# Performance work log

Hardware: AMD Instinct MI355X
Metric: run time of the kernel (lower is better)

Reference implementation:

```python
import jax, jax.numpy as jnp
import numpy as np

CODEBOOK_SIZE = 1024
LATENT_DIM = 64
BETA = 0.25      # commitment_beta
DECAY = 0.99     # ema_decay
EPS = 1e-5       # ema_eps
DIVERSITY_W = 1.0


def _hadamard(n):
    # Sylvester construction (n must be a power of 2)
    H = np.array([[1.0]], dtype=np.float32)
    while H.shape[0] < n:
        H = np.block([[H, H], [H, -H]])
    return H.astype(np.float32)


def setup_inputs() -> dict:
    key = jax.random.key(0)
    k1, k2, k3 = jax.random.split(key, 3)
    B, C, H, W = 32, LATENT_DIM, 32, 32
    x = jax.random.normal(k1, (B, C, H, W), dtype=jnp.float32)
    embedding_weight = jax.random.normal(k2, (CODEBOOK_SIZE, LATENT_DIM), dtype=jnp.float32)
    rotation_matrix = jnp.asarray(_hadamard(LATENT_DIM))
    ema_w = jax.random.normal(k3, (CODEBOOK_SIZE, LATENT_DIM), dtype=jnp.float32)
    ema_cluster_size = jnp.ones((CODEBOOK_SIZE,), dtype=jnp.float32)
    return {"x": x, "embedding_weight": embedding_weight,
            "rotation_matrix": rotation_matrix, "ema_w": ema_w,
            "ema_cluster_size": ema_cluster_size}


def reference(x, embedding_weight, rotation_matrix, ema_w, ema_cluster_size):
    B, C, H, W = x.shape
    K, D = embedding_weight.shape
    N = B * H * W
    sg = jax.lax.stop_gradient

    # flatten channel-last, rotate
    xf = jnp.transpose(x, (0, 2, 3, 1)).reshape(N, D)      # [N, D]
    xr = xf @ rotation_matrix                               # [N, D]

    # pairwise squared distances to codebook + argmin
    dist = (jnp.sum(xr * xr, axis=-1, keepdims=True)
            + jnp.sum(embedding_weight * embedding_weight, axis=-1)[None, :]
            - 2.0 * (xr @ embedding_weight.T))              # [N, K]
    idx = jnp.argmin(dist, axis=-1)                         # [N]

    # one-hot scatter equivalents (counts / dw) done with index scatter-add
    counts = jnp.zeros((K,), x.dtype).at[idx].add(1.0)      # encodings.sum(0)
    quant = embedding_weight[idx]                           # [N, D]
    # NOTE: original code views (B*H*W, C) row-major directly as (B, C, H, W)
    quant_out = quant.reshape(B, C, H, W)

    # EMA codebook update (training=True path)
    cs = ema_cluster_size * DECAY + (1.0 - DECAY) * counts
    n = jnp.sum(cs)
    cs = (cs + EPS) / (n + K * EPS) * n
    dw = jnp.zeros((K, D), x.dtype).at[idx].add(xr)         # encodings.T @ xr
    new_ema_w = ema_w * DECAY + (1.0 - DECAY) * dw
    new_embedding = new_ema_w / cs[:, None]

    commitment_loss = BETA * jnp.mean((sg(quant_out) - x) ** 2)
    codebook_loss = jnp.mean((quant_out - sg(x)) ** 2)

    # diversity: mean over ALL (i, j) pairs of ||e_i - xr_j||^2 (original
    # broadcasts (N,1,D) vs (N,D) -> (N,N,D)); identical closed form:
    e = new_embedding[idx]                                  # [N, D]
    diversity_loss = DIVERSITY_W * (jnp.mean(jnp.sum(e * e, axis=-1))
                                    + jnp.mean(jnp.sum(xr * xr, axis=-1))
                                    - 2.0 * jnp.dot(jnp.mean(e, axis=0), jnp.mean(xr, axis=0)))

    avg_probs = counts / N
    perplexity = jnp.exp(-jnp.sum(avg_probs * jnp.log(avg_probs + 1e-10)))

    quant_st = x + sg(quant_out - x)                        # straight-through
    return (quant_st, codebook_loss, commitment_loss, diversity_loss,
            perplexity, idx, cs, new_ema_w, new_embedding)
```

## Files before the change

kernel.cpp:

```cpp
#include <hip/hip_runtime.h>
#include <math.h>

#define NTOK 32768
#define KCB  1024
#define DIM  64
#define THETA 0.02f

typedef __attribute__((ext_vector_type(8))) short short8;
typedef __attribute__((ext_vector_type(4))) float f32x4;
#define MFMA __builtin_amdgcn_mfma_f32_16x16x32_bf16
#define ALOAD(p) __hip_atomic_load((p), __ATOMIC_RELAXED, __HIP_MEMORY_SCOPE_AGENT)

#define WS_XR      0
#define WS_ENORM   2097152
#define WS_EH      2098176
#define WS_EL      2130944
#define WS_COUNTS  2163712
#define WS_CS      2164736
#define WS_XRSUM   2165760
#define WS_ESUM    2166272
#define WS_SCALREP 2166784
#define WS_FLAGCNT 2166912
#define WS_IDX     2166928
#define WS_FLAG    2199696
#define WS_SORT    2232464
#define WS_OFF     2265232
#define WS_CUR     2266256

#define O_Q    0
#define O_CB   2097152
#define O_CM   2097153
#define O_DV   2097154
#define O_PP   2097155
#define O_IDX  2097156
#define O_CS   2129924
#define O_EW   2130948
#define O_EMB  2196484

__device__ __forceinline__ void hilo(float v, unsigned &h, unsigned &l)
{
    unsigned b  = __float_as_uint(v);
    unsigned hb = (b + 0x7FFFu + ((b >> 16) & 1u)) & 0xFFFF0000u;
    float lof   = v - __uint_as_float(hb);
    unsigned lb = __float_as_uint(lof);
    l = (lb + 0x7FFFu + ((lb >> 16) & 1u)) >> 16;
    h = hb >> 16;
}

__global__ __launch_bounds__(256) void k_rotate_enorm(const float* __restrict__ x,
    const float* __restrict__ E, float* __restrict__ xr, float* __restrict__ enorm,
    unsigned short* __restrict__ eh, unsigned short* __restrict__ el,
    float* __restrict__ counts, int* __restrict__ flagc)
{
    int tid = threadIdx.x;
    if (blockIdx.x >= 512) {
        int b = (int)blockIdx.x - 512;
        counts[(b << 8) + tid] = 0.f;
        if (b == 0 && tid < 16) flagc[tid] = 0;
        int k = (b << 8) + tid;
        const float* ep = E + ((size_t)k << 6);
        unsigned* ehw = (unsigned*)eh + (k << 5);
        unsigned* elw = (unsigned*)el + (k << 5);
        float s = 0.f;
        #pragma unroll
        for (int q = 0; q < 32; ++q) {
            float v0 = ep[2*q], v1 = ep[2*q+1];
            s = fmaf(v0, v0, s); s = fmaf(v1, v1, s);
            unsigned h0, l0, h1, l1;
            hilo(v0, h0, l0);
            hilo(v1, h1, l1);
            ehw[q] = h0 | (h1 << 16);
            elw[q] = l0 | (l1 << 16);
        }
        enorm[k] = s;
        return;
    }
    __shared__ float xt[64 * 65];
    int p  = blockIdx.x >> 4;
    int s0 = ((int)blockIdx.x & 15) << 6;

    {
        const float4* x4 = (const float4*)x;
        #pragma unroll
        for (int pass = 0; pass < 4; ++pass) {
            int q = (pass << 8) + tid;
            int c = q >> 4, col = (q & 15) << 2;
            float4 v = x4[(p << 14) + (c << 8) + (s0 >> 2) + (col >> 2)];
            float* dst = xt + c * 65 + col;
            dst[0] = v.x; dst[1] = v.y; dst[2] = v.z; dst[3] = v.w;
        }
    }
    __syncthreads();

    int lane = tid & 63, w = tid >> 6;
    #pragma unroll
    for (int i = 0; i < 4; ++i) {
        int sl = (w << 4) + (i << 2);
        const float* src = xt + lane * 65 + sl;
        float4 v = make_float4(src[0], src[1], src[2], src[3]);
        #pragma unroll
        for (int s = 1; s <= 32; s <<= 1) {
            float sgn = (lane & s) ? -1.f : 1.f;
            float ox = __shfl_xor(v.x, s);
            float oy = __shfl_xor(v.y, s);
            float oz = __shfl_xor(v.z, s);
            float ow = __shfl_xor(v.w, s);
            v.x = fmaf(sgn, v.x, ox);
            v.y = fmaf(sgn, v.y, oy);
            v.z = fmaf(sgn, v.z, oz);
            v.w = fmaf(sgn, v.w, ow);
        }
        int t0 = ((int)blockIdx.x << 6) + sl;
        float* dst = xr + ((size_t)t0 << 6) + lane;
        dst[0]   = v.x;
        dst[64]  = v.y;
        dst[128] = v.z;
        dst[192] = v.w;
    }
}

__global__ __launch_bounds__(256, 4) void k_argmin(const float* __restrict__ xr,
    const unsigned short* __restrict__ eh, const unsigned short* __restrict__ el,
    const float* __restrict__ enorm, int* __restrict__ idxw,
    float* __restrict__ out_idx, float* __restrict__ counts,
    int* __restrict__ flagcnt, int* __restrict__ flaglist)
{
    __shared__ uint4 ehs[1024];
    __shared__ uint4 els[1024];
    __shared__ float ens[128];
    __shared__ float m_b1[32], m_b2[32];
    __shared__ int   m_id[32];
    int tid = threadIdx.x;
    int lane = tid & 63, w = tid >> 6;
    int ts = w >> 1, kh = w & 1;
    int tx = lane & 15, gq = lane >> 4;
    int tokbase = ((int)blockIdx.x << 5) + (ts << 4);

    short8 ah0, al0, ah1, al1;
    {
        const float* xp = xr + ((size_t)(tokbase + tx) << 6) + (gq << 3);
        float4 xa = *(const float4*)(xp);
        float4 xb = *(const float4*)(xp + 4);
        float4 xc = *(const float4*)(xp + 32);
        float4 xd = *(const float4*)(xp + 36);
        float a0v[8] = {xa.x,xa.y,xa.z,xa.w,xb.x,xb.y,xb.z,xb.w};
        float a1v[8] = {xc.x,xc.y,xc.z,xc.w,xd.x,xd.y,xd.z,xd.w};
        #pragma unroll
        for (int j = 0; j < 8; ++j) {
            unsigned h, l;
            hilo(a0v[j], h, l);
            ah0[j] = (short)h; al0[j] = (short)l;
            hilo(a1v[j], h, l);
            ah1[j] = (short)h; al1[j] = (short)l;
        }
    }

    float b1[4], b2[4]; int idx[4];
    #pragma unroll
    for (int r = 0; r < 4; ++r) { b1[r] = 3.4e38f; b2[r] = 3.4e38f; idx[r] = 0; }

    int swz0 = gq ^ (tx & 7);
    int swz1 = (4 + gq) ^ (tx & 7);
    const f32x4 z4 = {0.f, 0.f, 0.f, 0.f};

    for (int ch = 0; ch < 8; ++ch) {
        int c0 = ch << 7;
        __syncthreads();
        {
            const uint4* ghs = (const uint4*)eh + ((size_t)c0 << 3);
            const uint4* gls = (const uint4*)el + ((size_t)c0 << 3);
            #pragma unroll
            for (int i = 0; i < 4; ++i) {
                int u = (i << 8) + tid;
                int rr = u >> 3, bb = u & 7;
                int bs = bb ^ (rr & 7);
                ehs[(rr << 3) + bs] = ghs[u];
                els[(rr << 3) + bs] = gls[u];
            }
            if (tid < 128) ens[tid] = enorm[c0 + tid];
        }
        __syncthreads();

        #pragma unroll
        for (int s = 0; s < 4; ++s) {
            int rbase = (kh << 6) + (s << 4) + tx;
            short8 bh0 = ((const short8*)ehs)[(rbase << 3) + swz0];
            short8 bh1 = ((const short8*)ehs)[(rbase << 3) + swz1];
            short8 bl0 = ((const short8*)els)[(rbase << 3) + swz0];
            short8 bl1 = ((const short8*)els)[(rbase << 3) + swz1];

            f32x4 a0 = MFMA(ah0, bh0, z4, 0, 0, 0);
            a0 = MFMA(ah0, bl0, a0, 0, 0, 0);
            a0 = MFMA(al0, bh0, a0, 0, 0, 0);
            f32x4 a1 = MFMA(ah1, bh1, z4, 0, 0, 0);
            a1 = MFMA(ah1, bl1, a1, 0, 0, 0);
            a1 = MFMA(al1, bh1, a1, 0, 0, 0);

            float en = ens[rbase];
            int kk = c0 + rbase;
            #pragma unroll
            for (int r = 0; r < 4; ++r) {
                float sv = fmaf(-2.f, a0[r], fmaf(-2.f, a1[r], en));
                float mx = fmaxf(sv, b1[r]);
                b2[r] = fminf(b2[r], mx);
                bool t = sv < b1[r];
                idx[r] = t ? kk : idx[r];
                b1[r] = fminf(b1[r], sv);
            }
        }
    }

    float v1f[4], v2f[4]; int idf[4];
    #pragma unroll
    for (int r = 0; r < 4; ++r) {
        float v1 = b1[r], v2 = b2[r]; int id = idx[r];
        #pragma unroll
        for (int m = 1; m <= 8; m <<= 1) {
            float o1 = __shfl_xor(v1, m);
            float o2 = __shfl_xor(v2, m);
            int   oi = __shfl_xor(id, m);
            float nb2 = fminf(fminf(v2, o2), fmaxf(v1, o1));
            bool t = (o1 < v1) || (o1 == v1 && oi < id);
            v1 = t ? o1 : v1;
            id = t ? oi : id;
            v2 = nb2;
        }
        v1f[r] = v1; v2f[r] = v2; idf[r] = id;
    }

    int tl = (ts << 4) + (gq << 2);
    if (kh == 1 && tx == 0) {
        #pragma unroll
        for (int r = 0; r < 4; ++r) {
            m_b1[tl + r] = v1f[r];
            m_b2[tl + r] = v2f[r];
            m_id[tl + r] = idf[r];
        }
    }
    __syncthreads();
    if (kh == 0 && tx == 0) {
        #pragma unroll
        for (int r = 0; r < 4; ++r) {
            float o1 = m_b1[tl + r], o2 = m_b2[tl + r];
            int   oi = m_id[tl + r];
            float v1 = v1f[r]; int id = idf[r];
            float b2m = fminf(fminf(v2f[r], o2), fmaxf(v1, o1));
            bool t = (o1 < v1) || (o1 == v1 && oi < id);
            float v1m = t ? o1 : v1;
            int   idm = t ? oi : id;
            int tok = tokbase + (gq << 2) + r;
            idxw[tok] = idm;
            out_idx[tok] = (float)idm;
            atomicAdd(&counts[idm], 1.f);
            if (b2m - v1m < THETA) {
                int pz = atomicAdd(flagcnt, 1);
                flaglist[pz] = tok;
            }
        }
    }
}

__global__ __launch_bounds__(256) void k_fixup_scan(const float* __restrict__ xr,
    const float* __restrict__ E, const float* __restrict__ enorm,
    const float* __restrict__ ecs,
    const int* __restrict__ flagcnt, const int* __restrict__ flaglist,
    int* __restrict__ idxw, float* __restrict__ out_idx, float* __restrict__ counts,
    float* __restrict__ out_cs, float* __restrict__ csw,
    int* __restrict__ off, int* __restrict__ cur, int* __restrict__ done_ctr,
    float* __restrict__ e_sum, float* __restrict__ xr_sum,
    float* __restrict__ scalrep)
{
    int tid = threadIdx.x;
    int lane = tid & 63;
    int wid = ((int)blockIdx.x * 256 + tid) >> 6;
    int cnt = flagcnt[0];
    for (int i = wid; i < cnt; i += 512) {
        int tok = flaglist[i];
        const float4* xp = (const float4*)(xr + ((size_t)tok << 6));
        float4 xa[16];
        #pragma unroll
        for (int q = 0; q < 16; ++q) xa[q] = xp[q];
        float best = 3.4e38f; int bidx = 0;
        for (int c = 0; c < 16; ++c) {
            int k = (c << 6) + lane;
            const float4* epp = (const float4*)(E + ((size_t)k << 6));
            float d = 0.f;
            #pragma unroll
            for (int q = 0; q < 16; ++q) {
                float4 e = epp[q];
                d = fmaf(xa[q].x, e.x, d);
                d = fmaf(xa[q].y, e.y, d);
                d = fmaf(xa[q].z, e.z, d);
                d = fmaf(xa[q].w, e.w, d);
            }
            float sv = fmaf(-2.f, d, enorm[k]);
            if (sv < best) { best = sv; bidx = k; }
        }
        #pragma unroll
        for (int m = 1; m <= 32; m <<= 1) {
            float ov = __shfl_xor(best, m);
            int   oi = __shfl_xor(bidx, m);
            if (ov < best || (ov == best && oi < bidx)) { best = ov; bidx = oi; }
        }
        if (lane == 0) {
            int old = idxw[tok];
            if (old != bidx) {
                atomicAdd(&counts[old], -1.f);
                atomicAdd(&counts[bidx], 1.f);
                idxw[tok] = bidx;
                out_idx[tok] = (float)bidx;
            }
        }
    }

    __shared__ int ticket;
    __syncthreads();
    if (tid == 0) ticket = atomicAdd(done_ctr, 1);
    __syncthreads();
    if (ticket != 127) return;

    e_sum[tid]       = 0.f;
    e_sum[256 + tid] = 0.f;
    xr_sum[tid]       = 0.f;
    xr_sum[256 + tid] = 0.f;
    if (tid < 128) scalrep[tid] = 0.f;
    if (tid == 0) done_ctr[1] = 0;

    __shared__ float wsum2[4];
    __shared__ int   wcnt2[4], woff2[4];
    __shared__ float nss;
    int w = tid >> 6;
    float cs4[4]; int ci4[4];
    int s = 0; float csum = 0.f;
    #pragma unroll
    for (int j = 0; j < 4; ++j) {
        int kk = (tid << 2) + j;
        float c = ALOAD(&counts[kk]);
        float cs = ecs[kk] * 0.99f + 0.01f * c;
        cs4[j] = cs;
        ci4[j] = (int)c;
        s += ci4[j];
        csum += cs;
    }
    int sc = s;
    #pragma unroll
    for (int o = 1; o < 64; o <<= 1) {
        int u = __shfl_up(sc, o);
        if (lane >= o) sc += u;
    }
    float v = csum;
    #pragma unroll
    for (int m = 32; m >= 1; m >>= 1) v += __shfl_xor(v, m);
    if (lane == 63) wcnt2[w] = sc;
    if (lane == 0)  wsum2[w] = v;
    __syncthreads();
    if (tid == 0) {
        int run = 0;
        #pragma unroll
        for (int i = 0; i < 4; ++i) { woff2[i] = run; run += wcnt2[i]; }
        nss = wsum2[0] + wsum2[1] + wsum2[2] + wsum2[3];
    }
    __syncthreads();
    float nn = nss;
    int run = woff2[w] + (sc - s);
    #pragma unroll
    for (int j = 0; j < 4; ++j) {
        int kk = (tid << 2) + j;
        off[kk] = run;
        cur[kk] = run;
        run += ci4[j];
        float csf = (cs4[j] + 1e-5f) / (nn + 1024.f * 1e-5f) * nn;
        out_cs[kk] = csf;
        csw[kk] = csf;
    }
}

__global__ __launch_bounds__(256) void k_quantscatter(const float* __restrict__ x,
    const float* __restrict__ E, const int* __restrict__ idxw,
    int* __restrict__ cur, int* __restrict__ sorted,
    float* __restrict__ outq, float* __restrict__ scalrep)
{
    __shared__ int lidx[32];
    __shared__ float wr[4], wn[4];
    int tid = threadIdx.x;
    int n0 = (int)blockIdx.x << 5;
    if (tid < 32) {
        int k = idxw[n0 + tid];
        lidx[tid] = k;
        int pos = atomicAdd(&cur[k], 1);
        sorted[pos] = n0 + tid;
    }
    __syncthreads();
    int f40 = (int)blockIdx.x << 9;
    float sq = 0.f, xn = 0.f;
    #pragma unroll
    for (int it = 0; it < 2; ++it) {
        int q = (it << 8) + tid;
        int kk = lidx[q >> 4];
        int d4 = q & 15;
        float4 xv = ((const float4*)x)[f40 + q];
        float4 ev = ((const float4*)E)[(kk << 4) + d4];
        float dx = ev.x - xv.x, dy = ev.y - xv.y, dz = ev.z - xv.z, dw_ = ev.w - xv.w;
        ((float4*)outq)[f40 + q] = make_float4(xv.x + dx, xv.y + dy, xv.z + dz, xv.w + dw_);
        sq += dx*dx + dy*dy + dz*dz + dw_*dw_;
        xn += xv.x*xv.x + xv.y*xv.y + xv.z*xv.z + xv.w*xv.w;
    }
    #pragma unroll
    for (int m = 32; m >= 1; m >>= 1) { sq += __shfl_xor(sq, m); xn += __shfl_xor(xn, m); }
    if ((tid & 63) == 0) { wr[tid >> 6] = sq; wn[tid >> 6] = xn; }
    __syncthreads();
    if (tid == 0) {
        int rep = ((int)blockIdx.x & 7) << 4;
        atomicAdd(&scalrep[rep + 0], wr[0] + wr[1] + wr[2] + wr[3]);
        atomicAdd(&scalrep[rep + 1], wn[0] + wn[1] + wn[2] + wn[3]);
    }
}

__global__ __launch_bounds__(256) void k_dwemb_final(const float* __restrict__ xr,
    const int* __restrict__ sorted, const int* __restrict__ off,
    const float* __restrict__ counts, const float* __restrict__ csw,
    const float* __restrict__ emaw, float* __restrict__ out_ew,
    float* __restrict__ out_emb, float* __restrict__ e_sum,
    float* __restrict__ scalrep, float* __restrict__ xr_sum,
    float* __restrict__ out, int* __restrict__ done_ctr)
{
    __shared__ float part[3][64];
    int k = blockIdx.x;
    int tid = threadIdx.x;
    int w = tid >> 6, d = tid & 63;
    int a = off[k];
    int cnt = (int)counts[k];
    int end = a + cnt;

    float sum = 0.f;
    for (int t = a + w; t < end; t += 4) {
        int tok = sorted[t];
        sum += xr[((size_t)tok << 6) + d];
    }
    if (w) part[w - 1][d] = sum;
    __syncthreads();
    if (w == 0) {
        float dw = sum + part[0][d] + part[1][d] + part[2][d];
        int i = (k << 6) + d;
        float nw = emaw[i] * 0.99f + 0.01f * dw;
        out_ew[i] = nw;
        float emb = nw / csw[k];
        out_emb[i] = emb;
        if (cnt > 0) {
            int rep = (k & 7) << 6;
            atomicAdd(&xr_sum[rep + d], dw);
            float c = (float)cnt;
            atomicAdd(&e_sum[rep + d], c * emb);
            float t2 = c * emb * emb;
            #pragma unroll
            for (int m = 32; m >= 1; m >>= 1) t2 += __shfl_xor(t2, m);
            if (d == 0) atomicAdd(&scalrep[((k & 7) << 4) + 2], t2);
        }
    }

    __shared__ int ticket;
    __syncthreads();
    if (tid == 0) ticket = atomicAdd(done_ctr, 1);
    __syncthreads();
    if (ticket != 1023) return;

    __shared__ float wt[4], wd[4];
    float tt = 0.f;
    #pragma unroll
    for (int j = 0; j < 4; ++j) {
        float aa = ALOAD(&counts[(tid << 2) + j]) * (1.f / 32768.f);
        tt += aa * logf(aa + 1e-10f);
    }
    float dc = 0.f;
    if (tid < 64) {
        float xs8 = 0.f, es8 = 0.f;
        #pragma unroll
        for (int r2 = 0; r2 < 8; ++r2) {
            xs8 += ALOAD(&xr_sum[(r2 << 6) + tid]);
            es8 += ALOAD(&e_sum[(r2 << 6) + tid]);
        }
        dc = es8 * xs8;
    }
    #pragma unroll
    for (int m = 32; m >= 1; m >>= 1) { tt += __shfl_xor(tt, m); dc += __shfl_xor(dc, m); }
    if ((tid & 63) == 0) { wt[w] = tt; wd[w] = dc; }
    __syncthreads();
    if (tid == 0) {
        float S = wt[0] + wt[1] + wt[2] + wt[3];
        float Dt = wd[0] + wd[1] + wd[2] + wd[3];
        float sqs = 0.f, xns = 0.f, s2s = 0.f;
        #pragma unroll
        for (int r2 = 0; r2 < 8; ++r2) {
            sqs += scalrep[(r2 << 4) + 0];
            xns += scalrep[(r2 << 4) + 1];
            s2s += ALOAD(&scalrep[(r2 << 4) + 2]);
        }
        float cb = sqs * (1.f / 2097152.f);
        out[O_CB] = cb;
        out[O_CM] = 0.25f * cb;
        float inv = 1.f / 32768.f;
        out[O_DV] = s2s * inv + 64.f * xns * inv - 2.f * (Dt * inv * inv);
        out[O_PP] = expf(-S);
    }
}

extern "C" void kernel_launch(void* const* d_in, const int* in_sizes, int n_in,
                              void* d_out, int out_size, void* d_ws, size_t ws_size,
                              hipStream_t stream)
{
    const float* x    = (const float*)d_in[0];
    const float* E    = (const float*)d_in[1];
    const float* emaw = (const float*)d_in[3];
    const float* ecs  = (const float*)d_in[4];
    float* out = (float*)d_out;
    float* ws  = (float*)d_ws;
    int* flagc = (int*)(ws + WS_FLAGCNT);

    hipLaunchKernelGGL(k_rotate_enorm, dim3(516), dim3(256), 0, stream,
                       x, E, ws + WS_XR, ws + WS_ENORM,
                       (unsigned short*)(ws + WS_EH), (unsigned short*)(ws + WS_EL),
                       ws + WS_COUNTS, flagc);
    hipLaunchKernelGGL(k_argmin, dim3(1024), dim3(256), 0, stream,
                       ws + WS_XR, (const unsigned short*)(ws + WS_EH),
                       (const unsigned short*)(ws + WS_EL), ws + WS_ENORM,
                       (int*)(ws + WS_IDX), out + O_IDX, ws + WS_COUNTS,
                       flagc, (int*)(ws + WS_FLAG));
    hipLaunchKernelGGL(k_fixup_scan, dim3(128), dim3(256), 0, stream,
                       ws + WS_XR, E, ws + WS_ENORM, ecs,
                       flagc, (const int*)(ws + WS_FLAG),
                       (int*)(ws + WS_IDX), out + O_IDX, ws + WS_COUNTS,
                       out + O_CS, ws + WS_CS,
                       (int*)(ws + WS_OFF), (int*)(ws + WS_CUR), flagc + 1,
                       ws + WS_ESUM, ws + WS_XRSUM, ws + WS_SCALREP);
    hipLaunchKernelGGL(k_quantscatter, dim3(1024), dim3(256), 0, stream,
                       x, E, (const int*)(ws + WS_IDX), (int*)(ws + WS_CUR),
                       (int*)(ws + WS_SORT), out + O_Q, ws + WS_SCALREP);
    hipLaunchKernelGGL(k_dwemb_final, dim3(1024), dim3(256), 0, stream,
                       ws + WS_XR, (const int*)(ws + WS_SORT),
                       (const int*)(ws + WS_OFF), ws + WS_COUNTS, ws + WS_CS,
                       emaw, out + O_EW, out + O_EMB, ws + WS_ESUM,
                       ws + WS_SCALREP, ws + WS_XRSUM, out, flagc + 2);
}
```

Before: 116.8 us.

## Fuse fixup with quantize and scatter with dw kernel, cutting launches

Argmin now writes a per-token flag array instead of atomically appending to a flag list. The fixup pass is folded into the per-32-token quantize kernel, and a last-block ticket computes the cluster-size scan. The counting-sort scatter moves into the dw/embedding kernel, guarded by a grid-wide spin barrier. Accumulator zeroing moves into the first kernel. The goal is to remove one kernel launch and the serial 128-block fixup phase. The cost is a spin barrier that assumes all 1024 blocks are resident at once, which risks deadlock or stalls.

```diff
diff --git a/kernel.cpp b/kernel.cpp
--- a/kernel.cpp
+++ b/kernel.cpp
@@ -50,13 +50,22 @@
 __global__ __launch_bounds__(256) void k_rotate_enorm(const float* __restrict__ x,
     const float* __restrict__ E, float* __restrict__ xr, float* __restrict__ enorm,
     unsigned short* __restrict__ eh, unsigned short* __restrict__ el,
-    float* __restrict__ counts, int* __restrict__ flagc)
+    float* __restrict__ counts, int* __restrict__ flagc,
+    float* __restrict__ e_sum, float* __restrict__ xr_sum,
+    float* __restrict__ scalrep)
 {
     int tid = threadIdx.x;
     if (blockIdx.x >= 512) {
         int b = (int)blockIdx.x - 512;
         counts[(b << 8) + tid] = 0.f;
-        if (b == 0 && tid < 16) flagc[tid] = 0;
+        if (b == 0) {
+            if (tid < 16) flagc[tid] = 0;
+            if (tid < 128) scalrep[tid] = 0.f;
+        } else if (b == 1) {
+            e_sum[tid] = 0.f; e_sum[256 + tid] = 0.f;
+        } else if (b == 2) {
+            xr_sum[tid] = 0.f; xr_sum[256 + tid] = 0.f;
+        }
         int k = (b << 8) + tid;
         const float* ep = E + ((size_t)k << 6);
         unsigned* ehw = (unsigned*)eh + (k << 5);
@@ -123,7 +132,7 @@
     const unsigned short* __restrict__ eh, const unsigned short* __restrict__ el,
     const float* __restrict__ enorm, int* __restrict__ idxw,
     float* __restrict__ out_idx, float* __restrict__ counts,
-    int* __restrict__ flagcnt, int* __restrict__ flaglist)
+    int* __restrict__ flag)
 {
     __shared__ uint4 ehs[1024];
     __shared__ uint4 els[1024];
@@ -252,30 +261,42 @@
             idxw[tok] = idm;
             out_idx[tok] = (float)idm;
             atomicAdd(&counts[idm], 1.f);
-            if (b2m - v1m < THETA) {
-                int pz = atomicAdd(flagcnt, 1);
-                flaglist[pz] = tok;
-            }
+            flag[tok] = (b2m - v1m < THETA) ? 1 : 0;
         }
     }
 }
 
-__global__ __launch_bounds__(256) void k_fixup_scan(const float* __restrict__ xr,
-    const float* __restrict__ E, const float* __restrict__ enorm,
-    const float* __restrict__ ecs,
-    const int* __restrict__ flagcnt, const int* __restrict__ flaglist,
-    int* __restrict__ idxw, float* __restrict__ out_idx, float* __restrict__ counts,
+__global__ __launch_bounds__(256) void k_fixupquant_scan(const float* __restrict__ x,
+    const float* __restrict__ xr, const float* __restrict__ E,
+    const float* __restrict__ enorm, const float* __restrict__ ecs,
+    const int* __restrict__ flag, int* __restrict__ idxw,
+    float* __restrict__ out_idx, float* __restrict__ counts,
     float* __restrict__ out_cs, float* __restrict__ csw,
     int* __restrict__ off, int* __restrict__ cur, int* __restrict__ done_ctr,
-    float* __restrict__ e_sum, float* __restrict__ xr_sum,
-    float* __restrict__ scalrep)
+    float* __restrict__ outq, float* __restrict__ scalrep)
 {
+    __shared__ int lidx[32];
+    __shared__ unsigned fmask;
+    __shared__ float wr[4], wn[4];
     int tid = threadIdx.x;
-    int lane = tid & 63;
-    int wid = ((int)blockIdx.x * 256 + tid) >> 6;
-    int cnt = flagcnt[0];
-    for (int i = wid; i < cnt; i += 512) {
-        int tok = flaglist[i];
+    int lane = tid & 63, w = tid >> 6;
+    int n0 = (int)blockIdx.x << 5;
+
+    int fl = 0;
+    if (tid < 32) {
+        lidx[tid] = idxw[n0 + tid];
+        fl = flag[n0 + tid];
+    }
+    unsigned long long bal = __ballot(fl != 0);
+    if (tid == 0) fmask = (unsigned)bal;
+    __syncthreads();
+
+    unsigned msk = fmask;
+    int widx = 0;
+    while (msk) {
+        int src = __ffs(msk) - 1; msk &= msk - 1;
+        if ((widx++ & 3) != w) continue;
+        int tok = n0 + src;
         const float4* xp = (const float4*)(xr + ((size_t)tok << 6));
         float4 xa[16];
         #pragma unroll
@@ -303,94 +324,18 @@
             if (ov < best || (ov == best && oi < bidx)) { best = ov; bidx = oi; }
         }
         if (lane == 0) {
-            int old = idxw[tok];
+            int old = lidx[src];
             if (old != bidx) {
                 atomicAdd(&counts[old], -1.f);
                 atomicAdd(&counts[bidx], 1.f);
+                lidx[src] = bidx;
                 idxw[tok] = bidx;
                 out_idx[tok] = (float)bidx;
             }
         }
     }
-
-    __shared__ int ticket;
-    __syncthreads();
-    if (tid == 0) ticket = atomicAdd(done_ctr, 1);
-    __syncthreads();
-    if (ticket != 127) return;
-
-    e_sum[tid]       = 0.f;
-    e_sum[256 + tid] = 0.f;
-    xr_sum[tid]       = 0.f;
-    xr_sum[256 + tid] = 0.f;
-    if (tid < 128) scalrep[tid] = 0.f;
-    if (tid == 0) done_ctr[1] = 0;
-
-    __shared__ float wsum2[4];
-    __shared__ int   wcnt2[4], woff2[4];
-    __shared__ float nss;
-    int w = tid >> 6;
-    float cs4[4]; int ci4[4];
-    int s = 0; float csum = 0.f;
-    #pragma unroll
-    for (int j = 0; j < 4; ++j) {
-        int kk = (tid << 2) + j;
-        float c = ALOAD(&counts[kk]);
-        float cs = ecs[kk] * 0.99f + 0.01f * c;
-        cs4[j] = cs;
-        ci4[j] = (int)c;
-        s += ci4[j];
-        csum += cs;
-    }
-    int sc = s;
-    #pragma unroll
-    for (int o = 1; o < 64; o <<= 1) {
-        int u = __shfl_up(sc, o);
-        if (lane >= o) sc += u;
-    }
-    float v = csum;
-    #pragma unroll
-    for (int m = 32; m >= 1; m >>= 1) v += __shfl_xor(v, m);
-    if (lane == 63) wcnt2[w] = sc;
-    if (lane == 0)  wsum2[w] = v;
-    __syncthreads();
-    if (tid == 0) {
-        int run = 0;
-        #pragma unroll
-        for (int i = 0; i < 4; ++i) { woff2[i] = run; run += wcnt2[i]; }
-        nss = wsum2[0] + wsum2[1] + wsum2[2] + wsum2[3];
-    }
-    __syncthreads();
-    float nn = nss;
-    int run = woff2[w] + (sc - s);
-    #pragma unroll
-    for (int j = 0; j < 4; ++j) {
-        int kk = (tid << 2) + j;
-        off[kk] = run;
-        cur[kk] = run;
-        run += ci4[j];
-        float csf = (cs4[j] + 1e-5f) / (nn + 1024.f * 1e-5f) * nn;
-        out_cs[kk] = csf;
-        csw[kk] = csf;
-    }
-}
-
-__global__ __launch_bounds__(256) void k_quantscatter(const float* __restrict__ x,
-    const float* __restrict__ E, const int* __restrict__ idxw,
-    int* __restrict__ cur, int* __restrict__ sorted,
-    float* __restrict__ outq, float* __restrict__ scalrep)
-{
-    __shared__ int lidx[32];
-    __shared__ float wr[4], wn[4];
-    int tid = threadIdx.x;
-    int n0 = (int)blockIdx.x << 5;
-    if (tid < 32) {
-        int k = idxw[n0 + tid];
-        lidx[tid] = k;
-        int pos = atomicAdd(&cur[k], 1);
-        sorted[pos] = n0 + tid;
-    }
-    __syncthreads();
+    __syncthreads();
+
     int f40 = (int)blockIdx.x << 9;
     float sq = 0.f, xn = 0.f;
     #pragma unroll
@@ -407,34 +352,103 @@
     }
     #pragma unroll
     for (int m = 32; m >= 1; m >>= 1) { sq += __shfl_xor(sq, m); xn += __shfl_xor(xn, m); }
-    if ((tid & 63) == 0) { wr[tid >> 6] = sq; wn[tid >> 6] = xn; }
+    if (lane == 0) { wr[w] = sq; wn[w] = xn; }
     __syncthreads();
     if (tid == 0) {
         int rep = ((int)blockIdx.x & 7) << 4;
         atomicAdd(&scalrep[rep + 0], wr[0] + wr[1] + wr[2] + wr[3]);
         atomicAdd(&scalrep[rep + 1], wn[0] + wn[1] + wn[2] + wn[3]);
     }
+
+    __shared__ int ticket;
+    __syncthreads();
+    if (tid == 0) ticket = atomicAdd(done_ctr, 1);
+    __syncthreads();
+    if (ticket != 1023) return;
+
+    __shared__ float wsum2[4];
+    __shared__ int   wcnt2[4], woff2[4];
+    __shared__ float nss;
+    float cs4[4]; int ci4[4];
+    int s = 0; float csum = 0.f;
+    #pragma unroll
+    for (int j = 0; j < 4; ++j) {
+        int kk = (tid << 2) + j;
+        float c = ALOAD(&counts[kk]);
+        float cs = ecs[kk] * 0.99f + 0.01f * c;
+        cs4[j] = cs;
+        ci4[j] = (int)c;
+        s += ci4[j];
+        csum += cs;
+    }
+    int sc = s;
+    #pragma unroll
+    for (int o = 1; o < 64; o <<= 1) {
+        int u = __shfl_up(sc, o);
+        if (lane >= o) sc += u;
+    }
+    float v = csum;
+    #pragma unroll
+    for (int m = 32; m >= 1; m >>= 1) v += __shfl_xor(v, m);
+    if (lane == 63) wcnt2[w] = sc;
+    if (lane == 0)  wsum2[w] = v;
+    __syncthreads();
+    if (tid == 0) {
+        int run = 0;
+        #pragma unroll
+        for (int i = 0; i < 4; ++i) { woff2[i] = run; run += wcnt2[i]; }
+        nss = wsum2[0] + wsum2[1] + wsum2[2] + wsum2[3];
+    }
+    __syncthreads();
+    float nn = nss;
+    int run = woff2[w] + (sc - s);
+    #pragma unroll
+    for (int j = 0; j < 4; ++j) {
+        int kk = (tid << 2) + j;
+        off[kk] = run;
+        cur[kk] = run;
+        run += ci4[j];
+        float csf = (cs4[j] + 1e-5f) / (nn + 1024.f * 1e-5f) * nn;
+        out_cs[kk] = csf;
+        csw[kk] = csf;
+    }
 }
 
-__global__ __launch_bounds__(256) void k_dwemb_final(const float* __restrict__ xr,
-    const int* __restrict__ sorted, const int* __restrict__ off,
-    const float* __restrict__ counts, const float* __restrict__ csw,
-    const float* __restrict__ emaw, float* __restrict__ out_ew,
-    float* __restrict__ out_emb, float* __restrict__ e_sum,
-    float* __restrict__ scalrep, float* __restrict__ xr_sum,
-    float* __restrict__ out, int* __restrict__ done_ctr)
+__global__ __launch_bounds__(256) void k_scatter_dwemb_final(
+    const float* __restrict__ xr, const int* __restrict__ idxw,
+    const int* __restrict__ off, const float* __restrict__ counts,
+    const float* __restrict__ csw, const float* __restrict__ emaw,
+    float* __restrict__ out_ew, float* __restrict__ out_emb,
+    float* __restrict__ e_sum, float* __restrict__ scalrep,
+    float* __restrict__ xr_sum, float* __restrict__ out,
+    int* __restrict__ cur, int* __restrict__ sorted,
+    int* __restrict__ spin_ctr, int* __restrict__ done_ctr)
 {
+    int tid = threadIdx.x;
+    int lane = tid & 63, w = tid >> 6;
+
+    int n0 = (int)blockIdx.x << 5;
+    if (tid < 32) {
+        int k = idxw[n0 + tid];
+        int pos = atomicAdd(&cur[k], 1);
+        atomicExch(&sorted[pos], n0 + tid);
+    }
+    __syncthreads();
+    if (tid == 0) {
+        atomicAdd(spin_ctr, 1);
+        while (ALOAD(spin_ctr) != 1024) __builtin_amdgcn_s_sleep(1);
+    }
+    __syncthreads();
+
     __shared__ float part[3][64];
     int k = blockIdx.x;
-    int tid = threadIdx.x;
-    int w = tid >> 6, d = tid & 63;
+    int d = lane;
     int a = off[k];
     int cnt = (int)counts[k];
     int end = a + cnt;
-
     float sum = 0.f;
     for (int t = a + w; t < end; t += 4) {
-        int tok = sorted[t];
+        int tok = ALOAD(&sorted[t]);
         sum += xr[((size_t)tok << 6) + d];
     }
     if (w) part[w - 1][d] = sum;
@@ -483,7 +497,7 @@
     }
     #pragma unroll
     for (int m = 32; m >= 1; m >>= 1) { tt += __shfl_xor(tt, m); dc += __shfl_xor(dc, m); }
-    if ((tid & 63) == 0) { wt[w] = tt; wd[w] = dc; }
+    if (lane == 0) { wt[w] = tt; wd[w] = dc; }
     __syncthreads();
     if (tid == 0) {
         float S = wt[0] + wt[1] + wt[2] + wt[3];
@@ -519,25 +533,24 @@
     hipLaunchKernelGGL(k_rotate_enorm, dim3(516), dim3(256), 0, stream,
                        x, E, ws + WS_XR, ws + WS_ENORM,
                        (unsigned short*)(ws + WS_EH), (unsigned short*)(ws + WS_EL),
-                       ws + WS_COUNTS, flagc);
+                       ws + WS_COUNTS, flagc,
+                       ws + WS_ESUM, ws + WS_XRSUM, ws + WS_SCALREP);
     hipLaunchKernelGGL(k_argmin, dim3(1024), dim3(256), 0, stream,
                        ws + WS_XR, (const unsigned short*)(ws + WS_EH),
                        (const unsigned short*)(ws + WS_EL), ws + WS_ENORM,
                        (int*)(ws + WS_IDX), out + O_IDX, ws + WS_COUNTS,
-                       flagc, (int*)(ws + WS_FLAG));
-    hipLaunchKernelGGL(k_fixup_scan, dim3(128), dim3(256), 0, stream,
-                       ws + WS_XR, E, ws + WS_ENORM, ecs,
-                       flagc, (const int*)(ws + WS_FLAG),
-                       (int*)(ws + WS_IDX), out + O_IDX, ws + WS_COUNTS,
-                       out + O_CS, ws + WS_CS,
+                       (int*)(ws + WS_FLAG));
+    hipLaunchKernelGGL(k_fixupquant_scan, dim3(1024), dim3(256), 0, stream,
+                       x, ws + WS_XR, E, ws + WS_ENORM, ecs,
+                       (const int*)(ws + WS_FLAG), (int*)(ws + WS_IDX),
+                       out + O_IDX, ws + WS_COUNTS, out + O_CS, ws + WS_CS,
                        (int*)(ws + WS_OFF), (int*)(ws + WS_CUR), flagc + 1,
-                       ws + WS_ESUM, ws + WS_XRSUM, ws + WS_SCALREP);
-    hipLaunchKernelGGL(k_quantscatter, dim3(1024), dim3(256), 0, stream,
-                       x, E, (const int*)(ws + WS_IDX), (int*)(ws + WS_CUR),
-                       (int*)(ws + WS_SORT), out + O_Q, ws + WS_SCALREP);
-    hipLaunchKernelGGL(k_dwemb_final, dim3(1024), dim3(256), 0, stream,
-                       ws + WS_XR, (const int*)(ws + WS_SORT),
+                       out + O_Q, ws + WS_SCALREP);
+    hipLaunchKernelGGL(k_scatter_dwemb_final, dim3(1024), dim3(256), 0, stream,
+                       ws + WS_XR, (const int*)(ws + WS_IDX),
                        (const int*)(ws + WS_OFF), ws + WS_COUNTS, ws + WS_CS,
                        emaw, out + O_EW, out + O_EMB, ws + WS_ESUM,
-                       ws + WS_SCALREP, ws + WS_XRSUM, out, flagc + 2);
+                       ws + WS_SCALREP, ws + WS_XRSUM, out,
+                       (int*)(ws + WS_CUR), (int*)(ws + WS_SORT),
+                       flagc + 2, flagc + 3);
 }
```

After: 143.6 us. 23.0% more time.
